# Optimization experiments

Hardware: AMD Instinct MI355X
Metric: run time of the kernel (lower is better)

The kernel has to match this reference:

```python
import jax, jax.numpy as jnp
import numpy as np

S, H, D, NL = 3, 64, 12, 2  # scales, hidden, input_dim, layers
B, L = 512, 512
EPS = 1e-5


def _layernorm(x, g, b):
    m = jnp.mean(x, axis=-1, keepdims=True)
    v = jnp.var(x, axis=-1, keepdims=True)
    return (x - m) * jax.lax.rsqrt(v + EPS) * g + b


def _cell(x_t, h, c, gw, gb, mi_w, mi_b, mo_w, mo_b, w1, b1, w2, b2, lag, lab, log, lob):
    # fused 4-gate linear: [B, in+H] @ [in+H, 4H]
    gates = jnp.concatenate([x_t, h], axis=-1) @ gw + gb
    f, i, g, o = jnp.split(gates, 4, axis=-1)
    c_new = jax.nn.sigmoid(f) * c + jax.nn.sigmoid(i) * jnp.tanh(g)
    h_t = jax.nn.sigmoid(o) * jnp.tanh(c_new)
    # MultiheadAttention with seq_len=1: softmax over one key == 1,
    # so attn_out = out_proj(v_proj(h_t)) exactly (q/k contribute nothing).
    v = h_t @ mi_w[:, 2 * H:] + mi_b[2 * H:]
    a = v @ mo_w + mo_b
    a = jax.nn.gelu(a @ w1 + b1, approximate=False) @ w2 + b2
    a = _layernorm(a, lag, lab)
    return _layernorm(a + h, log, lob), c_new


def _run_xlstm(xi, gw0, gb0, gw1, gb1, mi_w, mi_b, mo_w, mo_b,
               w1, b1, w2, b2, lag, lab, log, lob, rw0, rb0, rw1, rb1):
    # xi: [B, L, D] -> outputs [B, L, H]; 2-layer unidirectional xLSTM (eval: dropout=identity)
    Bb = xi.shape[0]
    z = jnp.zeros((Bb, H), xi.dtype)

    def step(carry, x_t):
        h0, c0, h1, c1 = carry
        h0, c0 = _cell(x_t, h0, c0, gw0, gb0, mi_w[0], mi_b[0], mo_w[0], mo_b[0],
                       w1[0], b1[0], w2[0], b2[0], lag[0], lab[0], log[0], lob[0])
        inp = h0 + x_t @ rw0 + rb0
        h1, c1 = _cell(inp, h1, c1, gw1, gb1, mi_w[1], mi_b[1], mo_w[1], mo_b[1],
                       w1[1], b1[1], w2[1], b2[1], lag[1], lab[1], log[1], lob[1])
        out = h1 + inp @ rw1 + rb1
        return (h0, c0, h1, c1), out

    _, ys = jax.lax.scan(step, (z, z, z, z), jnp.swapaxes(xi, 0, 1))
    return jnp.swapaxes(ys, 0, 1)


def _upsample_linear(xi, out_len):
    # F.interpolate(mode='linear', align_corners=False) on [B, Li, D] time axis
    Li = xi.shape[1]
    if Li == out_len:
        return xi
    sc = Li / out_len
    src = jnp.maximum((jnp.arange(out_len, dtype=jnp.float32) + 0.5) * sc - 0.5, 0.0)
    i0 = jnp.clip(jnp.floor(src).astype(jnp.int32), 0, Li - 1)
    i1 = jnp.minimum(i0 + 1, Li - 1)
    w = (src - i0.astype(jnp.float32))[None, :, None]
    return xi[:, i0] * (1.0 - w) + xi[:, i1] * w


def _forward(x, gw0, gb0, gw1, gb1, mi_w, mi_b, mo_w, mo_b, w1, b1, w2, b2,
             lag, lab, log, lob, rw0, rb0, rw1, rb1, attn_w):
    Ls = x.shape[1]
    ups = []
    for i in (1, 2, 3):
        start = Ls - Ls // i
        ups.append(_upsample_linear(x[:, start:, :], Ls))
    # bug-faithful ordering from source: xlstm[i] consumes upsampled_outputs[i-1]
    xs = jnp.stack([ups[2], ups[0], ups[1]], axis=0)  # [S, B, L, D]
    outs = jax.vmap(_run_xlstm)(xs, gw0, gb0, gw1, gb1, mi_w, mi_b, mo_w, mo_b,
                                w1, b1, w2, b2, lag, lab, log, lob,
                                rw0, rb0, rw1, rb1)      # [S, B, L, H]
    merged = jnp.moveaxis(outs, 0, 1)                    # [B, S, L, H]
    weights = jax.nn.softmax(merged @ attn_w, axis=1)    # softmax over scale dim
    return jnp.sum(merged * weights[..., None], axis=1)  # [B, L, H]


def setup_inputs() -> dict:
    key = jax.random.key(0)
    ks = iter(jax.random.split(key, 32))
    w = lambda *sh: jax.random.normal(next(ks), sh, jnp.float32) * 0.02
    IN0, IN1 = D + H, 2 * H
    return {
        'x': jax.random.normal(next(ks), (B, L, D), jnp.float32),
        'gw0': w(S, IN0, 4 * H), 'gb0': jnp.zeros((S, 4 * H)),
        'gw1': w(S, IN1, 4 * H), 'gb1': jnp.zeros((S, 4 * H)),
        'mi_w': w(S, NL, H, 3 * H), 'mi_b': jnp.zeros((S, NL, 3 * H)),
        'mo_w': w(S, NL, H, H), 'mo_b': jnp.zeros((S, NL, H)),
        'w1': w(S, NL, H, 2 * H), 'b1': jnp.zeros((S, NL, 2 * H)),
        'w2': w(S, NL, 2 * H, H), 'b2': jnp.zeros((S, NL, H)),
        'lag': jnp.ones((S, NL, H)), 'lab': jnp.zeros((S, NL, H)),
        'log': jnp.ones((S, NL, H)), 'lob': jnp.zeros((S, NL, H)),
        'rw0': w(S, D, H), 'rb0': jnp.zeros((S, H)),
        'rw1': w(S, H, H), 'rb1': jnp.zeros((S, H)),
        'attn_w': w(H),
    }


def reference(x, gw0, gb0, gw1, gb1, mi_w, mi_b, mo_w, mo_b, w1, b1, w2, b2,
              lag, lab, log, lob, rw0, rb0, rw1, rb1, attn_w):
    return _forward(x, gw0, gb0, gw1, gb1, mi_w, mi_b, mo_w, mo_b, w1, b1, w2, b2,
                    lag, lab, log, lob, rw0, rb0, rw1, rb1, attn_w)
```

## Files before the change

kernel.cpp:

```cpp
#include <hip/hip_runtime.h>
#include <hip/hip_bf16.h>
#include <math.h>

#define Sn 3
#define Hn 64
#define Dn 12
#define Bn 512
#define Ln 512
#define BC 4
#define IN0 76
#define NIN 22
#define CT 32
#define NCHUNK (Ln / CT)
#define P2OFF 0
#define P1OFF 384
#define GROFF 768
#define CBOFF 1026
#define MEGABLK 1538

#define NINP ((size_t)3 * Bn * CT * 64)
#define NG1R ((size_t)3 * Bn * CT * 320)
#define NMERG ((size_t)3 * Bn * CT * 64)

using bf16 = __hip_bfloat16;
typedef _Float16 h2 __attribute__((ext_vector_type(2)));
typedef _Float16 h4 __attribute__((ext_vector_type(4)));
typedef _Float16 h8t __attribute__((ext_vector_type(8)));

__device__ __forceinline__ float u2f(unsigned short x) {
    return __uint_as_float(((unsigned int)x) << 16);
}
__device__ __forceinline__ unsigned short f2u(float f) {
    bf16 h = __float2bfloat16(f);
    unsigned short u;
    __builtin_memcpy(&u, &h, 2);
    return u;
}

__device__ __forceinline__ float ex2(float x) {
#if __has_builtin(__builtin_amdgcn_exp2f)
    return __builtin_amdgcn_exp2f(x);
#else
    return exp2f(x);
#endif
}
__device__ __forceinline__ float frcp(float x) {
#if __has_builtin(__builtin_amdgcn_rcpf)
    return __builtin_amdgcn_rcpf(x);
#else
    return 1.0f / x;
#endif
}
__device__ __forceinline__ float sigm(float x) {
    return frcp(1.0f + ex2(-1.44269504f * x));
}
__device__ __forceinline__ float tanhfast(float x) {
    return 1.0f - 2.0f * frcp(1.0f + ex2(2.88539008f * x));
}
__device__ __forceinline__ float gelu_ex(float x) { return 0.5f * x * (1.0f + erff(x * 0.70710678118654752f)); }

__device__ __forceinline__ float fdot2f(h2 a, h2 b, float c) {
#if __has_builtin(__builtin_amdgcn_fdot2)
    return __builtin_amdgcn_fdot2(a, b, c, false);
#else
    return fmaf((float)a.x, (float)b.x, fmaf((float)a.y, (float)b.y, c));
#endif
}
__device__ __forceinline__ h2 cvt2(float x, float y) {
    h2 r; r.x = (_Float16)x; r.y = (_Float16)y; return r;
}
__device__ __forceinline__ void unpack8(h8t v, h2* out) {
    out[0] = __builtin_shufflevector(v, v, 0, 1);
    out[1] = __builtin_shufflevector(v, v, 2, 3);
    out[2] = __builtin_shufflevector(v, v, 4, 5);
    out[3] = __builtin_shufflevector(v, v, 6, 7);
}

template <int CTRL>
__device__ __forceinline__ float qp(float v) {
    return __int_as_float(__builtin_amdgcn_update_dpp(0, __float_as_int(v), CTRL, 0xF, 0xF, true));
}
__device__ __forceinline__ float qsum(float v) {
    v += qp<0xB1>(v);
    v += qp<0x4E>(v);
    return v;
}
__device__ __forceinline__ float osum(float v) {
    v = qsum(v);
    v += __int_as_float(__builtin_amdgcn_ds_swizzle(__float_as_int(v), 0x101F));
    return v;
}
__device__ __forceinline__ float redsum64(float v) {
    v += qp<0xB1>(v);
    v += qp<0x4E>(v);
    v += qp<0x141>(v);
    v += qp<0x140>(v);
    v += __int_as_float(__builtin_amdgcn_ds_swizzle(__float_as_int(v), 0x401F));
    v += __shfl_xor(v, 32, 64);
    return v;
}

__global__ __launch_bounds__(256) void detect_kernel(const unsigned short* __restrict__ xr,
                                                     int* __restrict__ flag) {
    __shared__ int sh[4];
    int tid = threadIdx.x;
    int cnt = 0;
    for (int i = tid; i < 2048; i += 256) {
        unsigned e = (xr[i] >> 7) & 0xFF;
        if (e >= 110 && e <= 133) cnt++;
    }
    for (int o = 32; o > 0; o >>= 1) cnt += __shfl_xor(cnt, o, 64);
    if ((tid & 63) == 0) sh[tid >> 6] = cnt;
    __syncthreads();
    if (tid == 0) {
        int tot = sh[0] + sh[1] + sh[2] + sh[3];
        *flag = (tot < 1640) ? 1 : 0;
    }
}

struct ConvArgs {
    const void* src[NIN];
    unsigned dstOff[NIN];
    unsigned n[NIN];
    unsigned blockStart[NIN + 1];
};

__global__ __launch_bounds__(256) void convert_kernel(ConvArgs a, float* __restrict__ dst,
                                                      const int* __restrict__ flag) {
    int bid = blockIdx.x;
    int i = 0;
    while (i < NIN - 1 && bid >= (int)a.blockStart[i + 1]) i++;
    unsigned lb = (unsigned)bid - a.blockStart[i];
    unsigned base = lb * 2048 + threadIdx.x;
    unsigned n = a.n[i];
    float* d = dst + a.dstOff[i];
    bool isf32 = (*flag != 0);
    const float* sf = (const float*)a.src[i];
    const unsigned short* su = (const unsigned short*)a.src[i];
#pragma unroll
    for (int e = 0; e < 8; e++) {
        unsigned idx = base + e * 256;
        if (idx < n) d[idx] = isf32 ? sf[idx] : u2f(su[idx]);
    }
}

__global__ __launch_bounds__(256) void fuse_kernel(
    const float* __restrict__ mi_w, const float* __restrict__ mi_b,
    const float* __restrict__ mo_w, const float* __restrict__ mo_b,
    const float* __restrict__ w1, const float* __restrict__ b1,
    float* __restrict__ M1out, float* __restrict__ bias1out) {
    int sl = blockIdx.x;
    __shared__ float T[64][64];
    __shared__ float bT[64];
    const float* Mv = mi_w + sl * 64 * 192;
    const float* Mo = mo_w + sl * 64 * 64;
    for (int idx = threadIdx.x; idx < 64 * 64; idx += 256) {
        int k = idx >> 6, n = idx & 63;
        float acc = 0.f;
        for (int j = 0; j < 64; j++) acc += Mv[k * 192 + 128 + j] * Mo[j * 64 + n];
        T[k][n] = acc;
    }
    for (int n = threadIdx.x; n < 64; n += 256) {
        float acc = mo_b[sl * 64 + n];
        for (int j = 0; j < 64; j++) acc += mi_b[sl * 192 + 128 + j] * Mo[j * 64 + n];
        bT[n] = acc;
    }
    __syncthreads();
    const float* W1 = w1 + sl * 64 * 128;
    for (int idx = threadIdx.x; idx < 64 * 128; idx += 256) {
        int k = idx >> 7, m = idx & 127;
        float acc = 0.f;
        for (int n = 0; n < 64; n++) acc += T[k][n] * W1[n * 128 + m];
        M1out[sl * 64 * 128 + idx] = acc;
    }
    for (int m = threadIdx.x; m < 128; m += 256) {
        float acc = b1[sl * 128 + m];
        for (int n = 0; n < 64; n++) acc += bT[n] * W1[n * 128 + m];
        bias1out[sl * 128 + m] = acc;
    }
}

__device__ __forceinline__ void pass1_body(
    int bid,
    const float* __restrict__ x, const float* __restrict__ gw0,
    const float* __restrict__ gb0,
    const float* __restrict__ M1g, const float* __restrict__ bias1g,
    const float* __restrict__ w2g, const float* __restrict__ b2g,
    const float* __restrict__ lag, const float* __restrict__ lab,
    const float* __restrict__ log_, const float* __restrict__ lob,
    const float* __restrict__ rw0, const float* __restrict__ rb0,
    float* __restrict__ gstate, _Float16* __restrict__ inp_w, int t0) {
    const int tid = threadIdx.x;
    const int sIdx = bid >> 7;
    const int gbase = (bid & 127) * BC;
    const int W = tid >> 6, lane = tid & 63;
    const int q = lane >> 2, ks = lane & 3;
    const int oct = lane >> 3, ks8 = lane & 7;
    const int j = W * 16 + q;
    const int cM = W * 32 + q * 2;
    const int uD = W * 16 + oct * 2;

    const int Li = (sIdx == 0) ? 170 : (sIdx == 1 ? 512 : 256);
    const int st = (sIdx == 0) ? 342 : (sIdx == 1 ? 0 : 256);
    const float sc = (float)Li / 512.0f;

    __shared__ float s_x[2][BC][12];
    __shared__ __align__(16) _Float16 s_h16[BC][72];
    __shared__ __align__(16) _Float16 s_ht16[BC][72];
    __shared__ __align__(16) _Float16 s_z16[BC][136];
    __shared__ float s_t2[BC][64];
    __shared__ float s_rw0[768];

    __builtin_amdgcn_s_setprio(1);

    const float* gw0s = gw0 + sIdx * IN0 * 256;
    float wx[12];
    h2 wg16[4][8], wm16[2][8], ww16[2][8];
#pragma unroll
    for (int g = 0; g < 4; g++)
#pragma unroll
        for (int d = 0; d < 3; d++) wx[g * 3 + d] = gw0s[(ks * 3 + d) * 256 + j + 64 * g];
#pragma unroll
    for (int g = 0; g < 4; g++)
#pragma unroll
        for (int kk = 0; kk < 8; kk++)
            wg16[g][kk] = cvt2(gw0s[(12 + ks * 16 + 2 * kk) * 256 + j + 64 * g],
                               gw0s[(12 + ks * 16 + 2 * kk + 1) * 256 + j + 64 * g]);
    const float* M1s = M1g + (sIdx * 2 + 0) * 8192;
#pragma unroll
    for (int cc = 0; cc < 2; cc++)
#pragma unroll
        for (int kk = 0; kk < 8; kk++)
            wm16[cc][kk] = cvt2(M1s[(ks * 16 + 2 * kk) * 128 + cM + cc],
                                M1s[(ks * 16 + 2 * kk + 1) * 128 + cM + cc]);
    const float* w2s = w2g + (sIdx * 2 + 0) * 8192;
#pragma unroll
    for (int cc = 0; cc < 2; cc++)
#pragma unroll
        for (int kk = 0; kk < 8; kk++)
            ww16[cc][kk] = cvt2(w2s[(ks8 * 16 + 2 * kk) * 64 + uD + cc],
                                w2s[(ks8 * 16 + 2 * kk + 1) * 64 + uD + cc]);

    float h_gb[4];
#pragma unroll
    for (int g = 0; g < 4; g++) h_gb[g] = gb0[sIdx * 256 + j + 64 * g];
    float h_b1[2] = {bias1g[(sIdx * 2 + 0) * 128 + cM], bias1g[(sIdx * 2 + 0) * 128 + cM + 1]};
    float h_b2[2] = {b2g[(sIdx * 2 + 0) * 64 + uD], b2g[(sIdx * 2 + 0) * 64 + uD + 1]};
    int ei = (sIdx * 2 + 0) * 64 + lane;
    float eLag = lag[ei], eLab = lab[ei], eLog = log_[ei], eLob = lob[ei];
    float eRb0 = rb0[sIdx * 64 + lane];

    for (int i = tid; i < 768; i += 256) s_rw0[i] = rw0[sIdx * 768 + i];
    {
        int b = tid >> 6, jj = tid & 63;
        float hv = (t0 == 0) ? 0.f : gstate[((size_t)(sIdx * Bn + gbase + b)) * 256 + jj];
        s_h16[b][jj] = (_Float16)hv;
    }
    float cS = (t0 == 0) ? 0.f
                         : gstate[((size_t)(sIdx * Bn + gbase + ks)) * 256 + 64 + j];
    if (tid < BC * 12) {
        int b = tid / 12, d = tid % 12;
        float srcp = fmaxf((t0 + 0.5f) * sc - 0.5f, 0.f);
        int i0 = (int)floorf(srcp); if (i0 > Li - 1) i0 = Li - 1;
        int i1 = i0 + 1; if (i1 > Li - 1) i1 = Li - 1;
        float w = srcp - (float)i0;
        int gb = gbase + b;
        s_x[0][b][d] = x[(gb * Ln + st + i0) * 12 + d] * (1.0f - w) + x[(gb * Ln + st + i1) * 12 + d] * w;
    }
    __syncthreads();

    for (int tt = 0; tt < CT; tt++) {
        const int sl = tt & 1;
        float myF = 0, myI = 0, myG = 0, myO = 0;
#pragma unroll
        for (int b = 0; b < BC; b++) {
            const h8t* hp = (const h8t*)&s_h16[b][ks * 16];
            h8t hv0 = hp[0], hv1 = hp[1];
            h2 hk[8];
            unpack8(hv0, hk); unpack8(hv1, hk + 4);
            float x0 = s_x[sl][b][ks * 3], x1 = s_x[sl][b][ks * 3 + 1], x2 = s_x[sl][b][ks * 3 + 2];
            float acc[4];
#pragma unroll
            for (int g = 0; g < 4; g++) {
                float s0 = (ks == 0) ? h_gb[g] : 0.f;
                acc[g] = fmaf(wx[g * 3], x0, fmaf(wx[g * 3 + 1], x1, fmaf(wx[g * 3 + 2], x2, s0)));
            }
#pragma unroll
            for (int kk = 0; kk < 8; kk++) {
#pragma unroll
                for (int g = 0; g < 4; g++)
                    acc[g] = fdot2f(wg16[g][kk], hk[kk], acc[g]);
            }
            float a0 = qsum(acc[0]);
            float a1 = qsum(acc[1]);
            float a2 = qsum(acc[2]);
            float a3 = qsum(acc[3]);
            if (ks == b) { myF = a0; myI = a1; myG = a2; myO = a3; }
        }
        {
            float cn = sigm(myF) * cS + sigm(myI) * tanhfast(myG);
            cS = cn;
            s_ht16[ks][j] = (_Float16)(sigm(myO) * tanhfast(cn));
        }
        __syncthreads();
        float z0 = 0, z1 = 0;
#pragma unroll
        for (int b = 0; b < BC; b++) {
            const h8t* hp = (const h8t*)&s_ht16[b][ks * 16];
            h8t hv0 = hp[0], hv1 = hp[1];
            h2 hk[8];
            unpack8(hv0, hk); unpack8(hv1, hk + 4);
            float acc0 = (ks == 0) ? h_b1[0] : 0.f;
            float acc1 = (ks == 0) ? h_b1[1] : 0.f;
#pragma unroll
            for (int kk = 0; kk < 8; kk++) {
                acc0 = fdot2f(wm16[0][kk], hk[kk], acc0);
                acc1 = fdot2f(wm16[1][kk], hk[kk], acc1);
            }
            float a0 = qsum(acc0);
            float a1 = qsum(acc1);
            if (ks == b) { z0 = a0; z1 = a1; }
        }
        *(h2*)&s_z16[ks][cM] = cvt2(gelu_ex(z0), gelu_ex(z1));
        __syncthreads();
#pragma unroll
        for (int b = 0; b < BC; b++) {
            const h8t* zp = (const h8t*)&s_z16[b][ks8 * 16];
            h8t zv0 = zp[0], zv1 = zp[1];
            h2 zk[8];
            unpack8(zv0, zk); unpack8(zv1, zk + 4);
            float acc0 = (ks8 == 0) ? h_b2[0] : 0.f;
            float acc1 = (ks8 == 0) ? h_b2[1] : 0.f;
#pragma unroll
            for (int kk = 0; kk < 8; kk++) {
                acc0 = fdot2f(ww16[0][kk], zk[kk], acc0);
                acc1 = fdot2f(ww16[1][kk], zk[kk], acc1);
            }
            float a0 = osum(acc0);
            float a1 = osum(acc1);
            if (ks8 == b) { s_t2[b][uD] = a0; s_t2[b][uD + 1] = a1; }
        }
        __syncthreads();
        {
            const int bb = W;
            float v = s_t2[bb][lane];
            float m = redsum64(v) * (1.0f / 64.0f);
            float var = redsum64(v * v) * (1.0f / 64.0f) - m * m;
            float rs = rsqrtf(fmaxf(var, 0.0f) + 1e-5f);
            float a = (v - m) * rs * eLag + eLab;
            float hOld = (float)s_h16[bb][lane];
            float y = a + hOld;
            float m2 = redsum64(y) * (1.0f / 64.0f);
            float var2 = redsum64(y * y) * (1.0f / 64.0f) - m2 * m2;
            float rs2 = rsqrtf(fmaxf(var2, 0.0f) + 1e-5f);
            float h0n = (y - m2) * rs2 * eLog + eLob;
            s_h16[bb][lane] = (_Float16)h0n;
            float p = h0n + eRb0;
#pragma unroll
            for (int d = 0; d < 12; d++)
                p = fmaf(s_x[sl][bb][d], s_rw0[d * 64 + lane], p);
            inp_w[(((size_t)(sIdx * Bn + gbase + bb)) * CT + tt) * 64 + lane] = (_Float16)p;
            if (tt + 1 < CT && lane < 12) {
                int d = lane;
                int t = t0 + tt + 1;
                float srcp = fmaxf((t + 0.5f) * sc - 0.5f, 0.f);
                int i0 = (int)floorf(srcp); if (i0 > Li - 1) i0 = Li - 1;
                int i1 = i0 + 1; if (i1 > Li - 1) i1 = Li - 1;
                float w = srcp - (float)i0;
                int gb = gbase + bb;
                s_x[sl ^ 1][bb][d] = x[(gb * Ln + st + i0) * 12 + d] * (1.0f - w) +
                                     x[(gb * Ln + st + i1) * 12 + d] * w;
            }
        }
        __syncthreads();
    }
    {
        int b = tid >> 6, jj = tid & 63;
        gstate[((size_t)(sIdx * Bn + gbase + b)) * 256 + jj] = (float)s_h16[b][jj];
    }
    gstate[((size_t)(sIdx * Bn + gbase + ks)) * 256 + 64 + j] = cS;
}

__device__ __forceinline__ void pass2_body(
    int bid,
    const float* __restrict__ gw1,
    const float* __restrict__ M1g, const float* __restrict__ bias1g,
    const float* __restrict__ w2g, const float* __restrict__ b2g,
    const float* __restrict__ lag, const float* __restrict__ lab,
    const float* __restrict__ log_, const float* __restrict__ lob,
    const _Float16* __restrict__ G1Rr, float* __restrict__ gstate,
    unsigned short* __restrict__ merged_w, int t0) {
    const int tid = threadIdx.x;
    const int sIdx = bid >> 7;
    const int gbase = (bid & 127) * BC;
    const int W = tid >> 6, lane = tid & 63;
    const int q = lane >> 2, ks = lane & 3;
    const int oct = lane >> 3, ks8 = lane & 7;
    const int j = W * 16 + q;
    const int cM = W * 32 + q * 2;
    const int uD = W * 16 + oct * 2;

    __shared__ __align__(16) _Float16 p2_h16[BC][72];
    __shared__ __align__(16) _Float16 p2_ht16[BC][72];
    __shared__ __align__(16) _Float16 p2_z16[BC][136];
    __shared__ float p2_t2[BC][64];

    __builtin_amdgcn_s_setprio(1);

    const float* gw1s = gw1 + (size_t)sIdx * 128 * 256;
    h2 wg16[4][8], wm16[2][8], ww16[2][8];
#pragma unroll
    for (int g = 0; g < 4; g++)
#pragma unroll
        for (int kk = 0; kk < 8; kk++)
            wg16[g][kk] = cvt2(gw1s[(64 + ks * 16 + 2 * kk) * 256 + j + 64 * g],
                               gw1s[(64 + ks * 16 + 2 * kk + 1) * 256 + j + 64 * g]);
    const float* M1s = M1g + (sIdx * 2 + 1) * 8192;
#pragma unroll
    for (int cc = 0; cc < 2; cc++)
#pragma unroll
        for (int kk = 0; kk < 8; kk++)
            wm16[cc][kk] = cvt2(M1s[(ks * 16 + 2 * kk) * 128 + cM + cc],
                                M1s[(ks * 16 + 2 * kk + 1) * 128 + cM + cc]);
    const float* w2s = w2g + (sIdx * 2 + 1) * 8192;
#pragma unroll
    for (int cc = 0; cc < 2; cc++)
#pragma unroll
        for (int kk = 0; kk < 8; kk++)
            ww16[cc][kk] = cvt2(w2s[(ks8 * 16 + 2 * kk) * 64 + uD + cc],
                                w2s[(ks8 * 16 + 2 * kk + 1) * 64 + uD + cc]);

    float h_b1[2] = {bias1g[(sIdx * 2 + 1) * 128 + cM], bias1g[(sIdx * 2 + 1) * 128 + cM + 1]};
    float h_b2[2] = {b2g[(sIdx * 2 + 1) * 64 + uD], b2g[(sIdx * 2 + 1) * 64 + uD + 1]};
    int ei = (sIdx * 2 + 1) * 64 + lane;
    float eLag = lag[ei], eLab = lab[ei], eLog = log_[ei], eLob = lob[ei];

    {
        int b = tid >> 6, jj = tid & 63;
        float hv = (t0 == 0) ? 0.f : gstate[((size_t)(sIdx * Bn + gbase + b)) * 256 + 128 + jj];
        p2_h16[b][jj] = (_Float16)hv;
    }
    float cS = (t0 == 0) ? 0.f
                         : gstate[((size_t)(sIdx * Bn + gbase + ks)) * 256 + 192 + j];
    __syncthreads();

    const size_t rowBase = ((size_t)(sIdx * Bn + gbase)) * CT;

    for (int tt = 0; tt < CT; tt++) {
        float g1rv[BC];
#pragma unroll
        for (int b = 0; b < BC; b++)
            g1rv[b] = (float)G1Rr[(rowBase + (size_t)b * CT + tt) * 320 + ks * 64 + j];
        float myF = 0, myI = 0, myG = 0, myO = 0;
#pragma unroll
        for (int b = 0; b < BC; b++) {
            const h8t* hp = (const h8t*)&p2_h16[b][ks * 16];
            h8t hv0 = hp[0], hv1 = hp[1];
            h2 hk[8];
            unpack8(hv0, hk); unpack8(hv1, hk + 4);
            float acc[4];
#pragma unroll
            for (int g = 0; g < 4; g++) acc[g] = (ks == g) ? g1rv[b] : 0.f;
#pragma unroll
            for (int kk = 0; kk < 8; kk++) {
#pragma unroll
                for (int g = 0; g < 4; g++)
                    acc[g] = fdot2f(wg16[g][kk], hk[kk], acc[g]);
            }
            float a0 = qsum(acc[0]);
            float a1 = qsum(acc[1]);
            float a2 = qsum(acc[2]);
            float a3 = qsum(acc[3]);
            if (ks == b) { myF = a0; myI = a1; myG = a2; myO = a3; }
        }
        {
            float cn = sigm(myF) * cS + sigm(myI) * tanhfast(myG);
            cS = cn;
            p2_ht16[ks][j] = (_Float16)(sigm(myO) * tanhfast(cn));
        }
        __syncthreads();
        float z0 = 0, z1 = 0;
#pragma unroll
        for (int b = 0; b < BC; b++) {
            const h8t* hp = (const h8t*)&p2_ht16[b][ks * 16];
            h8t hv0 = hp[0], hv1 = hp[1];
            h2 hk[8];
            unpack8(hv0, hk); unpack8(hv1, hk + 4);
            float acc0 = (ks == 0) ? h_b1[0] : 0.f;
            float acc1 = (ks == 0) ? h_b1[1] : 0.f;
#pragma unroll
            for (int kk = 0; kk < 8; kk++) {
                acc0 = fdot2f(wm16[0][kk], hk[kk], acc0);
                acc1 = fdot2f(wm16[1][kk], hk[kk], acc1);
            }
            float a0 = qsum(acc0);
            float a1 = qsum(acc1);
            if (ks == b) { z0 = a0; z1 = a1; }
        }
        *(h2*)&p2_z16[ks][cM] = cvt2(gelu_ex(z0), gelu_ex(z1));
        __syncthreads();
#pragma unroll
        for (int b = 0; b < BC; b++) {
            const h8t* zp = (const h8t*)&p2_z16[b][ks8 * 16];
            h8t zv0 = zp[0], zv1 = zp[1];
            h2 zk[8];
            unpack8(zv0, zk); unpack8(zv1, zk + 4);
            float acc0 = (ks8 == 0) ? h_b2[0] : 0.f;
            float acc1 = (ks8 == 0) ? h_b2[1] : 0.f;
#pragma unroll
            for (int kk = 0; kk < 8; kk++) {
                acc0 = fdot2f(ww16[0][kk], zk[kk], acc0);
                acc1 = fdot2f(ww16[1][kk], zk[kk], acc1);
            }
            float a0 = osum(acc0);
            float a1 = osum(acc1);
            if (ks8 == b) { p2_t2[b][uD] = a0; p2_t2[b][uD + 1] = a1; }
        }
        __syncthreads();
        {
            const int bb = W;
            float r = (float)G1Rr[(rowBase + (size_t)bb * CT + tt) * 320 + 256 + lane];
            float v = p2_t2[bb][lane];
            float m = redsum64(v) * (1.0f / 64.0f);
            float var = redsum64(v * v) * (1.0f / 64.0f) - m * m;
            float rs = rsqrtf(fmaxf(var, 0.0f) + 1e-5f);
            float a = (v - m) * rs * eLag + eLab;
            float hOld = (float)p2_h16[bb][lane];
            float y = a + hOld;
            float m2 = redsum64(y) * (1.0f / 64.0f);
            float var2 = redsum64(y * y) * (1.0f / 64.0f) - m2 * m2;
            float rs2 = rsqrtf(fmaxf(var2, 0.0f) + 1e-5f);
            float h1n = (y - m2) * rs2 * eLog + eLob;
            p2_h16[bb][lane] = (_Float16)h1n;
            merged_w[(((size_t)(sIdx * Bn + gbase + bb)) * CT + tt) * 64 + lane] = f2u(h1n + r);
        }
        __syncthreads();
    }
    {
        int b = tid >> 6, jj = tid & 63;
        gstate[((size_t)(sIdx * Bn + gbase + b)) * 256 + 128 + jj] = (float)p2_h16[b][jj];
    }
    gstate[((size_t)(sIdx * Bn + gbase + ks)) * 256 + 192 + j] = cS;
}

__device__ __forceinline__ void g1r_body(
    int bid,
    const float* __restrict__ gw1, const float* __restrict__ gb1,
    const float* __restrict__ rw1, const float* __restrict__ rb1,
    const _Float16* __restrict__ inp_r, _Float16* __restrict__ G1Rw) {
    const int tid = threadIdx.x;
    const int s = bid / 86;
    const int bb = bid % 86;
    __shared__ __align__(16) float s_inT[64][36];

    const int c4 = tid & 63, rg = tid >> 6;
    float4 bias = *(const float4*)(gb1 + s * 256 + c4 * 4);
    float rbias = rb1[s * 64 + c4];
    const float* Wg = gw1 + (size_t)s * 128 * 256;
    const float* Wr = rw1 + (size_t)s * 64 * 64;

    const size_t sRow = (size_t)s * Bn * CT;
    for (int tile = 0; tile < 6; tile++) {
        int tIdx = bb * 6 + tile;
        if (tIdx >= 512) break;
        int r0 = tIdx * 32;
        __syncthreads();
        for (int i = tid; i < 512; i += 256) {
            int r = i >> 4, kq = i & 15;
            h4 v = *(const h4*)(inp_r + (sRow + r0 + r) * 64 + kq * 4);
            s_inT[kq * 4 + 0][r] = (float)v.x;
            s_inT[kq * 4 + 1][r] = (float)v.y;
            s_inT[kq * 4 + 2][r] = (float)v.z;
            s_inT[kq * 4 + 3][r] = (float)v.w;
        }
        __syncthreads();
        float acc[8][4], accR[8];
#pragma unroll
        for (int r = 0; r < 8; r++) {
            acc[r][0] = bias.x; acc[r][1] = bias.y; acc[r][2] = bias.z; acc[r][3] = bias.w;
            accR[r] = rbias;
        }
#pragma unroll 4
        for (int k = 0; k < 64; k++) {
            float4 w = *(const float4*)(Wg + (size_t)k * 256 + c4 * 4);
            float wR = Wr[k * 64 + c4];
            float4 iA = *(const float4*)&s_inT[k][rg * 8];
            float4 iB = *(const float4*)&s_inT[k][rg * 8 + 4];
            float in8[8] = {iA.x, iA.y, iA.z, iA.w, iB.x, iB.y, iB.z, iB.w};
#pragma unroll
            for (int r = 0; r < 8; r++) {
                acc[r][0] = fmaf(in8[r], w.x, acc[r][0]);
                acc[r][1] = fmaf(in8[r], w.y, acc[r][1]);
                acc[r][2] = fmaf(in8[r], w.z, acc[r][2]);
                acc[r][3] = fmaf(in8[r], w.w, acc[r][3]);
                accR[r] = fmaf(in8[r], wR, accR[r]);
            }
        }
#pragma unroll
        for (int r = 0; r < 8; r++) {
            size_t row = sRow + r0 + rg * 8 + r;
            h4 o;
            o.x = (_Float16)acc[r][0]; o.y = (_Float16)acc[r][1];
            o.z = (_Float16)acc[r][2]; o.w = (_Float16)acc[r][3];
            *(h4*)(G1Rw + row * 320 + c4 * 4) = o;
            G1Rw[row * 320 + 256 + c4] = (_Float16)accR[r];
        }
    }
}

__device__ __forceinline__ void combine_body(
    int bid,
    const unsigned short* __restrict__ merged_r,
    const float* __restrict__ attn_w,
    void* __restrict__ outv, const int* __restrict__ flag, int t0) {
    int W = threadIdx.x >> 6, lane = threadIdx.x & 63;
    float aw = attn_w[lane];
    size_t stride = (size_t)Bn * CT * 64;
    int isf = *flag;
#pragma unroll
    for (int r = 0; r < 8; r++) {
        int wid = (bid * 4 + W) * 8 + r;
        int b = wid >> 5, tt = wid & 31;
        size_t base = (((size_t)b) * CT + tt) * 64 + lane;
        float m0 = u2f(merged_r[base]);
        float m1 = u2f(merged_r[base + stride]);
        float m2 = u2f(merged_r[base + 2 * stride]);
        float e0 = redsum64(m0 * aw);
        float e1 = redsum64(m1 * aw);
        float e2 = redsum64(m2 * aw);
        float mx = fmaxf(e0, fmaxf(e1, e2));
        float x0 = expf(e0 - mx), x1 = expf(e1 - mx), x2 = expf(e2 - mx);
        float inv = 1.0f / (x0 + x1 + x2);
        float val = (x0 * m0 + x1 * m1 + x2 * m2) * inv;
        size_t ob = (((size_t)b) * Ln + t0 + tt) * 64 + lane;
        if (isf) ((float*)outv)[ob] = val;
        else ((unsigned short*)outv)[ob] = f2u(val);
    }
}

__global__ __launch_bounds__(256) __attribute__((amdgpu_waves_per_eu(4, 4)))
void mega_kernel(
    const float* __restrict__ x, const float* __restrict__ gw0,
    const float* __restrict__ gb0, const float* __restrict__ gw1,
    const float* __restrict__ gb1,
    const float* __restrict__ M1g, const float* __restrict__ bias1g,
    const float* __restrict__ w2g, const float* __restrict__ b2g,
    const float* __restrict__ lag, const float* __restrict__ lab,
    const float* __restrict__ log_, const float* __restrict__ lob,
    const float* __restrict__ rw0, const float* __restrict__ rb0,
    const float* __restrict__ rw1, const float* __restrict__ rb1,
    float* __restrict__ gstate,
    _Float16* __restrict__ inpB, _Float16* __restrict__ G1RB,
    unsigned short* __restrict__ mergedB,
    const float* __restrict__ attn_w, void* __restrict__ outv,
    const int* __restrict__ flag,
    int c_p1, int c_g1r, int c_p2, int c_comb) {
    int bid = blockIdx.x;
    if (bid < P1OFF) {
        if (c_p2 >= 0) {
            const _Float16* g1r_r = G1RB + (size_t)(c_p2 & 1) * NG1R;
            unsigned short* merged_w = mergedB + (size_t)(c_p2 & 1) * NMERG;
            pass2_body(bid, gw1, M1g, bias1g, w2g, b2g, lag, lab, log_, lob,
                       g1r_r, gstate, merged_w, c_p2 * CT);
        }
    } else if (bid < GROFF) {
        if (c_p1 >= 0) {
            _Float16* inp_w = inpB + (size_t)(c_p1 & 1) * NINP;
            pass1_body(bid - P1OFF, x, gw0, gb0, M1g, bias1g, w2g, b2g,
                       lag, lab, log_, lob, rw0, rb0, gstate, inp_w, c_p1 * CT);
        }
    } else if (bid < CBOFF) {
        if (c_g1r >= 0) {
            const _Float16* inp_r = inpB + (size_t)(c_g1r & 1) * NINP;
            _Float16* g1r_w = G1RB + (size_t)(c_g1r & 1) * NG1R;
            g1r_body(bid - GROFF, gw1, gb1, rw1, rb1, inp_r, g1r_w);
        }
    } else {
        if (c_comb >= 0) {
            const unsigned short* merged_r = mergedB + (size_t)(c_comb & 1) * NMERG;
            combine_body(bid - CBOFF, merged_r, attn_w, outv, flag, c_comb * CT);
        }
    }
}

extern "C" void kernel_launch(void* const* d_in, const int* in_sizes, int n_in,
                              void* d_out, int out_size, void* d_ws, size_t ws_size,
                              hipStream_t stream) {
    (void)out_size; (void)ws_size;
    int* flag = (int*)d_ws;
    float* canon = (float*)((char*)d_ws + 16);

    ConvArgs ca;
    size_t tot = 0;
    unsigned nblocks = 0;
    for (int i = 0; i < NIN; i++) {
        ca.src[i] = d_in[i];
        ca.dstOff[i] = (unsigned)tot;
        unsigned n = (unsigned)in_sizes[i];
        ca.n[i] = n;
        ca.blockStart[i] = nblocks;
        nblocks += (n + 2047) / 2048;
        tot += n;
    }
    ca.blockStart[NIN] = nblocks;

    size_t canonBytes = (tot * 4 + 15) & ~(size_t)15;
    char* p = (char*)d_ws + 16 + canonBytes;
    float* M1 = (float*)p;       p += (size_t)3 * 2 * 64 * 128 * 4;
    float* bias1 = (float*)p;    p += (size_t)3 * 2 * 128 * 4;
    float* gstate = (float*)p;   p += (size_t)3 * 512 * 256 * 4;
    p = (char*)(((uintptr_t)p + 15) & ~(uintptr_t)15);
    _Float16* inpB = (_Float16*)p;      p += 2 * NINP * 2;
    _Float16* G1RB = (_Float16*)p;      p += 2 * NG1R * 2;
    p = (char*)(((uintptr_t)p + 15) & ~(uintptr_t)15);
    unsigned short* mergedB = (unsigned short*)p;

    const float* x    = canon + ca.dstOff[0];
    const float* gw0  = canon + ca.dstOff[1];
    const float* gb0  = canon + ca.dstOff[2];
    const float* gw1  = canon + ca.dstOff[3];
    const float* gb1  = canon + ca.dstOff[4];
    const float* mi_w = canon + ca.dstOff[5];
    const float* mi_b = canon + ca.dstOff[6];
    const float* mo_w = canon + ca.dstOff[7];
    const float* mo_b = canon + ca.dstOff[8];
    const float* w1   = canon + ca.dstOff[9];
    const float* b1   = canon + ca.dstOff[10];
    const float* w2   = canon + ca.dstOff[11];
    const float* b2   = canon + ca.dstOff[12];
    const float* lag  = canon + ca.dstOff[13];
    const float* lab  = canon + ca.dstOff[14];
    const float* log_ = canon + ca.dstOff[15];
    const float* lob  = canon + ca.dstOff[16];
    const float* rw0  = canon + ca.dstOff[17];
    const float* rb0  = canon + ca.dstOff[18];
    const float* rw1  = canon + ca.dstOff[19];
    const float* rb1  = canon + ca.dstOff[20];
    const float* attn_w = canon + ca.dstOff[21];

    detect_kernel<<<dim3(1), dim3(256), 0, stream>>>((const unsigned short*)d_in[0], flag);
    convert_kernel<<<dim3(nblocks), dim3(256), 0, stream>>>(ca, canon, flag);
    fuse_kernel<<<dim3(6), dim3(256), 0, stream>>>(mi_w, mi_b, mo_w, mo_b, w1, b1, M1, bias1);

    for (int m = 0; m <= NCHUNK + 2; m++) {
        int c1 = (m < NCHUNK) ? m : -1;
        int cg = (m - 1 >= 0 && m - 1 < NCHUNK) ? m - 1 : -1;
        int c2 = (m - 2 >= 0 && m - 2 < NCHUNK) ? m - 2 : -1;
        int cc = (m - 3 >= 0 && m - 3 < NCHUNK) ? m - 3 : -1;
        mega_kernel<<<dim3(MEGABLK), dim3(256), 0, stream>>>(
            x, gw0, gb0, gw1, gb1, M1, bias1, w2, b2, lag, lab, log_, lob,
            rw0, rb0, rw1, rb1, gstate, inpB, G1RB, mergedB, attn_w, d_out, flag,
            c1, cg, c2, cc);
    }
}
```

Measured before the change: 3.517 ms.

## Permute layer-1 gate weights for coalesced loads and prefetch next timestep inputs

Adds a one-time permutation kernel that reorders the layer-1 gate weight columns and biases, so the precomputed gate inputs are laid out contiguously per thread (W*64+lane) instead of strided by gate. The pass-2 recurrence loop now prefetches the next timestep's precomputed gate and residual values before the barrier, hiding global load latency behind compute. The occupancy hint is loosened from 4 waves to 2-3 per EU, giving more registers for the prefetch buffers at the cost of fewer resident waves. The permuted layout must match the lane-to-gate mapping exactly or the results will be wrong.

After: 3.520 ms. Within noise of the previous version (+0.1%).

```diff
diff --git a/kernel.cpp b/kernel.cpp
--- a/kernel.cpp
+++ b/kernel.cpp
@@ -177,6 +177,22 @@
         float acc = b1[sl * 128 + m];
         for (int n = 0; n < 64; n++) acc += bT[n] * W1[n * 128 + m];
         bias1out[sl * 128 + m] = acc;
+    }
+}
+
+__global__ __launch_bounds__(256) void perm_kernel(
+    const float* __restrict__ gw1, const float* __restrict__ gb1,
+    float* __restrict__ gw1p, float* __restrict__ gb1p) {
+    int s = blockIdx.x;
+    int tid = threadIdx.x;
+    for (int idx = tid; idx < 64 * 256; idx += 256) {
+        int k = idx >> 8, p = idx & 255;
+        int c = (p & 3) * 64 + ((p >> 6) << 4) + ((p >> 2) & 15);
+        gw1p[((size_t)s * 64 + k) * 256 + p] = gw1[(size_t)s * 128 * 256 + k * 256 + c];
+    }
+    for (int p = tid; p < 256; p += 256) {
+        int c = (p & 3) * 64 + ((p >> 6) << 4) + ((p >> 2) & 15);
+        gb1p[s * 256 + p] = gb1[s * 256 + c];
     }
 }
 
@@ -445,12 +461,15 @@
     __syncthreads();
 
     const size_t rowBase = ((size_t)(sIdx * Bn + gbase)) * CT;
+    const int pOff = W * 64 + lane;
+
+    float g1rv[BC], rv;
+#pragma unroll
+    for (int b = 0; b < BC; b++)
+        g1rv[b] = (float)G1Rr[(rowBase + (size_t)b * CT) * 320 + pOff];
+    rv = (float)G1Rr[(rowBase + (size_t)W * CT) * 320 + 256 + lane];
 
     for (int tt = 0; tt < CT; tt++) {
-        float g1rv[BC];
-#pragma unroll
-        for (int b = 0; b < BC; b++)
-            g1rv[b] = (float)G1Rr[(rowBase + (size_t)b * CT + tt) * 320 + ks * 64 + j];
         float myF = 0, myI = 0, myG = 0, myO = 0;
 #pragma unroll
         for (int b = 0; b < BC; b++) {
@@ -477,6 +496,17 @@
             float cn = sigm(myF) * cS + sigm(myI) * tanhfast(myG);
             cS = cn;
             p2_ht16[ks][j] = (_Float16)(sigm(myO) * tanhfast(cn));
+        }
+        float g1rn[BC], rn;
+        if (tt + 1 < CT) {
+#pragma unroll
+            for (int b = 0; b < BC; b++)
+                g1rn[b] = (float)G1Rr[(rowBase + (size_t)b * CT + tt + 1) * 320 + pOff];
+            rn = (float)G1Rr[(rowBase + (size_t)W * CT + tt + 1) * 320 + 256 + lane];
+        } else {
+#pragma unroll
+            for (int b = 0; b < BC; b++) g1rn[b] = 0.f;
+            rn = 0.f;
         }
         __syncthreads();
         float z0 = 0, z1 = 0;
@@ -519,7 +549,6 @@
         __syncthreads();
         {
             const int bb = W;
-            float r = (float)G1Rr[(rowBase + (size_t)bb * CT + tt) * 320 + 256 + lane];
             float v = p2_t2[bb][lane];
             float m = redsum64(v) * (1.0f / 64.0f);
             float var = redsum64(v * v) * (1.0f / 64.0f) - m * m;
@@ -532,9 +561,12 @@
             float rs2 = rsqrtf(fmaxf(var2, 0.0f) + 1e-5f);
             float h1n = (y - m2) * rs2 * eLog + eLob;
             p2_h16[bb][lane] = (_Float16)h1n;
-            merged_w[(((size_t)(sIdx * Bn + gbase + bb)) * CT + tt) * 64 + lane] = f2u(h1n + r);
-        }
-        __syncthreads();
+            merged_w[(((size_t)(sIdx * Bn + gbase + bb)) * CT + tt) * 64 + lane] = f2u(h1n + rv);
+        }
+        __syncthreads();
+#pragma unroll
+        for (int b = 0; b < BC; b++) g1rv[b] = g1rn[b];
+        rv = rn;
     }
     {
         int b = tid >> 6, jj = tid & 63;
@@ -545,7 +577,7 @@
 
 __device__ __forceinline__ void g1r_body(
     int bid,
-    const float* __restrict__ gw1, const float* __restrict__ gb1,
+    const float* __restrict__ gw1p, const float* __restrict__ gb1p,
     const float* __restrict__ rw1, const float* __restrict__ rb1,
     const _Float16* __restrict__ inp_r, _Float16* __restrict__ G1Rw) {
     const int tid = threadIdx.x;
@@ -554,9 +586,9 @@
     __shared__ __align__(16) float s_inT[64][36];
 
     const int c4 = tid & 63, rg = tid >> 6;
-    float4 bias = *(const float4*)(gb1 + s * 256 + c4 * 4);
+    float4 bias = *(const float4*)(gb1p + s * 256 + c4 * 4);
     float rbias = rb1[s * 64 + c4];
-    const float* Wg = gw1 + (size_t)s * 128 * 256;
+    const float* Wg = gw1p + (size_t)s * 64 * 256;
     const float* Wr = rw1 + (size_t)s * 64 * 64;
 
     const size_t sRow = (size_t)s * Bn * CT;
@@ -638,11 +670,11 @@
     }
 }
 
-__global__ __launch_bounds__(256) __attribute__((amdgpu_waves_per_eu(4, 4)))
+__global__ __launch_bounds__(256) __attribute__((amdgpu_waves_per_eu(2, 3)))
 void mega_kernel(
     const float* __restrict__ x, const float* __restrict__ gw0,
     const float* __restrict__ gb0, const float* __restrict__ gw1,
-    const float* __restrict__ gb1,
+    const float* __restrict__ gw1p, const float* __restrict__ gb1p,
     const float* __restrict__ M1g, const float* __restrict__ bias1g,
     const float* __restrict__ w2g, const float* __restrict__ b2g,
     const float* __restrict__ lag, const float* __restrict__ lab,
@@ -673,7 +705,7 @@
         if (c_g1r >= 0) {
             const _Float16* inp_r = inpB + (size_t)(c_g1r & 1) * NINP;
             _Float16* g1r_w = G1RB + (size_t)(c_g1r & 1) * NG1R;
-            g1r_body(bid - GROFF, gw1, gb1, rw1, rb1, inp_r, g1r_w);
+            g1r_body(bid - GROFF, gw1p, gb1p, rw1, rb1, inp_r, g1r_w);
         }
     } else {
         if (c_comb >= 0) {
@@ -708,6 +740,8 @@
     char* p = (char*)d_ws + 16 + canonBytes;
     float* M1 = (float*)p;       p += (size_t)3 * 2 * 64 * 128 * 4;
     float* bias1 = (float*)p;    p += (size_t)3 * 2 * 128 * 4;
+    float* gw1p = (float*)p;     p += (size_t)3 * 64 * 256 * 4;
+    float* gb1p = (float*)p;     p += (size_t)3 * 256 * 4;
     float* gstate = (float*)p;   p += (size_t)3 * 512 * 256 * 4;
     p = (char*)(((uintptr_t)p + 15) & ~(uintptr_t)15);
     _Float16* inpB = (_Float16*)p;      p += 2 * NINP * 2;
@@ -741,6 +775,7 @@
     detect_kernel<<<dim3(1), dim3(256), 0, stream>>>((const unsigned short*)d_in[0], flag);
     convert_kernel<<<dim3(nblocks), dim3(256), 0, stream>>>(ca, canon, flag);
     fuse_kernel<<<dim3(6), dim3(256), 0, stream>>>(mi_w, mi_b, mo_w, mo_b, w1, b1, M1, bias1);
+    perm_kernel<<<dim3(3), dim3(256), 0, stream>>>(gw1, gb1, gw1p, gb1p);
 
     for (int m = 0; m <= NCHUNK + 2; m++) {
         int c1 = (m < NCHUNK) ? m : -1;
@@ -748,7 +783,7 @@
         int c2 = (m - 2 >= 0 && m - 2 < NCHUNK) ? m - 2 : -1;
         int cc = (m - 3 >= 0 && m - 3 < NCHUNK) ? m - 3 : -1;
         mega_kernel<<<dim3(MEGABLK), dim3(256), 0, stream>>>(
-            x, gw0, gb0, gw1, gb1, M1, bias1, w2, b2, lag, lab, log_, lob,
+            x, gw0, gb0, gw1, gw1p, gb1p, M1, bias1, w2, b2, lag, lab, log_, lob,
             rw0, rb0, rw1, rb1, gstate, inpB, G1RB, mergedB, attn_w, d_out, flag,
             c1, cg, c2, cc);
     }
```
